# Kernel tuning notes

Measured on AMD Instinct MI355X. Metric: run time of the kernel, lower is better.

## Reference

```python
import jax, jax.numpy as jnp
import numpy as np

B, DIM, MID, H, W = 4, 256, 128, 128, 128
EPS = 1e-5


def _conv(x, w, pad):
    # x: [B,C,H,W], w: [O,I,k,k]
    return jax.lax.conv_general_dilated(
        x, w, window_strides=(1, 1), padding=[(pad, pad), (pad, pad)],
        dimension_numbers=('NCHW', 'OIHW', 'NCHW'))


def _bn(x, g, b, m, v):
    inv = jax.lax.rsqrt(v + EPS)
    scale = (g * inv)[None, :, None, None]
    shift = (b - m * g * inv)[None, :, None, None]
    return x * scale + shift


def _convbnrelu(x, w, g, b, m, v):
    return jax.nn.relu(_bn(_conv(x, w, 1), g, b, m, v))


# CornerNet directional pools: sequential max-accumulation scans.
def top_pool(x):     # max over y' >= y  -> reversed cummax along H
    return jax.lax.cummax(x, axis=2, reverse=True)

def bottom_pool(x):  # max over y' <= y
    return jax.lax.cummax(x, axis=2)

def left_pool(x):    # max over x' >= x
    return jax.lax.cummax(x, axis=3, reverse=True)

def right_pool(x):   # max over x' <= x
    return jax.lax.cummax(x, axis=3)


def setup_inputs() -> dict:
    key = jax.random.key(0)
    ks = jax.random.split(key, 32)
    it = iter(ks)

    def w(shape, scale=0.05):
        return jax.random.normal(next(it), shape, jnp.float32) * scale

    def bn_params(c):
        return (jnp.ones((c,), jnp.float32) + 0.1 * jax.random.normal(next(it), (c,), jnp.float32),
                0.1 * jax.random.normal(next(it), (c,), jnp.float32),
                0.1 * jax.random.normal(next(it), (c,), jnp.float32),
                jax.random.uniform(next(it), (c,), jnp.float32) + 0.5)

    inp = {'x': jax.random.normal(next(it), (B, DIM, H, W), jnp.float32)}

    inp['p1_w'] = w((MID, DIM, 3, 3))
    inp['p1_g'], inp['p1_b'], inp['p1_m'], inp['p1_v'] = bn_params(MID)
    inp['p2_w'] = w((MID, DIM, 3, 3))
    inp['p2_g'], inp['p2_b'], inp['p2_m'], inp['p2_v'] = bn_params(MID)
    inp['p_w'] = w((DIM, MID, 3, 3))
    inp['p_g'], inp['p_b'], inp['p_m'], inp['p_v'] = bn_params(DIM)
    inp['c1_w'] = w((DIM, DIM, 1, 1))
    inp['c1_g'], inp['c1_b'], inp['c1_m'], inp['c1_v'] = bn_params(DIM)
    inp['c2_w'] = w((DIM, DIM, 3, 3))
    inp['c2_g'], inp['c2_b'], inp['c2_m'], inp['c2_v'] = bn_params(DIM)
    return inp


def reference(x,
              p1_w, p1_g, p1_b, p1_m, p1_v,
              p2_w, p2_g, p2_b, p2_m, p2_v,
              p_w, p_g, p_b, p_m, p_v,
              c1_w, c1_g, c1_b, c1_m, c1_v,
              c2_w, c2_g, c2_b, c2_m, c2_v):
    # branch 1: conv-bn-relu -> top pool -> bottom pool
    pool1 = bottom_pool(top_pool(_convbnrelu(x, p1_w, p1_g, p1_b, p1_m, p1_v)))
    # branch 2: conv-bn-relu -> left pool -> right pool
    pool2 = right_pool(left_pool(_convbnrelu(x, p2_w, p2_g, p2_b, p2_m, p2_v)))
    # merge branch
    p_bn1 = _bn(_conv(pool1 + pool2, p_w, 1), p_g, p_b, p_m, p_v)
    # skip branch: 1x1 conv + bn
    bn1 = _bn(_conv(x, c1_w, 0), c1_g, c1_b, c1_m, c1_v)
    # residual add + relu, then final conv-bn-relu
    return _convbnrelu(jax.nn.relu(p_bn1 + bn1), c2_w, c2_g, c2_b, c2_m, c2_v)
```

## Files before the change

### kernel.cpp

```cpp
#include <hip/hip_runtime.h>
#include <hip/hip_bf16.h>
#include <math.h>


constexpr int NB   = 4;
constexpr int CDIM = 256;
constexpr int CMID = 128;
constexpr int HS   = 128;
constexpr int WS   = 128;
constexpr float EPS = 1e-5f;

typedef __bf16 bf16x8 __attribute__((ext_vector_type(8)));
typedef float  f32x4  __attribute__((ext_vector_type(4)));

#define AS1 __attribute__((address_space(1)))
#define AS3 __attribute__((address_space(3)))

__device__ __forceinline__ void load16_lds(const void* gsrc, void* ldst) {
    __builtin_amdgcn_global_load_lds((const AS1 unsigned int*)gsrc,
                                     (AS3 unsigned int*)ldst, 16, 0, 0);
}

__global__ __launch_bounds__(512) void k_xprep(const float* __restrict__ xin,
                                               __hip_bfloat16* __restrict__ Xc)
{
    const int y = blockIdx.x;
    const int b = blockIdx.y;
    const int t = threadIdx.x;
    __shared__ __hip_bfloat16 lds[128 * 264];
#pragma unroll
    for (int k = 0; k < 16; ++k) {
        int idx = t + k * 512;
        int ci = idx >> 5, x4 = idx & 31;
        f32x4 v = *(const f32x4*)(xin + (((size_t)b * CDIM + ci) * HS + y) * WS + x4 * 4);
#pragma unroll
        for (int j = 0; j < 4; ++j)
            lds[(x4 * 4 + j) * 264 + ci] = __float2bfloat16(v[j]);
    }
    __syncthreads();
#pragma unroll
    for (int k = 0; k < 8; ++k) {
        int i = t + k * 512;
        int x = i >> 5, c8 = i & 31;
        bf16x8 vv = *(const bf16x8*)(lds + x * 264 + c8 * 8);
        *(bf16x8*)(Xc + ((size_t)(b * 128 + y) * 128 + x) * 256 + c8 * 8) = vv;
    }
}

__global__ __launch_bounds__(256) void k_wprep_all(
    const float* __restrict__ p1w, const float* __restrict__ p2w,
    const float* __restrict__ c2w, const float* __restrict__ c1w,
    __hip_bfloat16* __restrict__ Aw1, __hip_bfloat16* __restrict__ Aw2,
    __hip_bfloat16* __restrict__ Aw5, __hip_bfloat16* __restrict__ Aw4,
    f32x4* __restrict__ zdst)
{
    const int bid = blockIdx.x;
    const int t   = threadIdx.x;
    if (bid < 512) {
        const float* W; __hip_bfloat16* A; int co;
        if (bid < 128)      { W = p1w; A = Aw1; co = bid; }
        else if (bid < 256) { W = p2w; A = Aw2; co = bid - 128; }
        else                { W = c2w; A = Aw5; co = bid - 256; }
#pragma unroll
        for (int tap = 0; tap < 9; ++tap)
            A[(size_t)co * 2304 + tap * 256 + t] =
                __float2bfloat16(W[((size_t)co * CDIM + t) * 9 + tap]);
    } else if (bid < 640) {
        int base = (bid - 512) * 512 + t;
        Aw4[base]       = __float2bfloat16(c1w[base]);
        Aw4[base + 256] = __float2bfloat16(c1w[base + 256]);
    } else if (bid < 768) {
        zdst[(size_t)(bid - 640) * 256 + t] = (f32x4){0.f, 0.f, 0.f, 0.f};
    } else {
        if (t < 16) zdst[32768 + t] = (f32x4){0.f, 0.f, 0.f, 0.f};
    }
}

template<int MODE>
__global__ __launch_bounds__(512, 2) void k_conv3(
    const __hip_bfloat16* __restrict__ Xc,
    const __hip_bfloat16* __restrict__ AwA, const __hip_bfloat16* __restrict__ AwB,
    const float* __restrict__ zbuf,
    const float* __restrict__ g1, const float* __restrict__ b1,
    const float* __restrict__ m1, const float* __restrict__ v1,
    const float* __restrict__ g2, const float* __restrict__ b2,
    const float* __restrict__ m2, const float* __restrict__ v2,
    float* __restrict__ out0, unsigned* __restrict__ cmax,
    unsigned* __restrict__ rmax, int CO)
{
    const int y0     = blockIdx.x * 4;
    const int branch = blockIdx.y;
    const int b      = blockIdx.z;
    const int co0    = (MODE == 0) ? branch * 128 : 0;

    const __hip_bfloat16* Aw = (MODE == 1 && branch) ? AwB : AwA;
    const float* gg  = (MODE == 1 && branch) ? g2 : g1;
    const float* bbp = (MODE == 1 && branch) ? b2 : b1;
    const float* mmp = (MODE == 1 && branch) ? m2 : m1;
    const float* vvp = (MODE == 1 && branch) ? v2 : v1;

    constexpr int BUFB = 904 * 64;
    __shared__ alignas(16) char smb[2 * BUFB];
    __shared__ float s_sc[128], s_sh[128];
    __shared__ unsigned s_red[4][128];

    const int t    = threadIdx.x;
    const int lane = t & 63;
    const int w    = t >> 6;
    const int ml   = lane & 15;
    const int q    = lane >> 4;
    const int yy    = w >> 1;
    const int mbase = (w & 1) * 64;

    if (t < 128) {
        int co = co0 + t;
        float iv = rsqrtf(vvp[co] + EPS);
        float sc = gg[co] * iv;
        s_sc[t] = sc;
        s_sh[t] = bbp[co] - mmp[co] * sc;
    }
    if (MODE == 1 && branch == 1) ((unsigned*)s_red)[t] = 0u;

    f32x4 acc[4][8];
#pragma unroll
    for (int mt = 0; mt < 4; ++mt)
#pragma unroll
        for (int nt = 0; nt < 8; ++nt)
            acc[mt][nt] = (f32x4){0.f, 0.f, 0.f, 0.f};

    const __hip_bfloat16* bbase = Xc + (size_t)(b * 128) * 128 * 256;

    auto stage_slot = [&](int p, int nky, int ncih, char* dst) {
        int i = t + p * 512;
        if (i < 3616) {
            int row = i >> 2, sl = i & 3;
            int c = sl ^ ((row >> 1) & 3);
            const __hip_bfloat16* src;
            if (row < 384) {
                int jj = row >> 7, col = row & 127;
                src = Aw + (size_t)(co0 + col) * 2304 + (3 * nky + jj) * 256
                         + ncih * 32 + c * 8;
            } else {
                int rbi = row - 384;
                int yl  = rbi / 130;
                int xi  = rbi - 130 * yl;
                int gy  = y0 + nky - 1 + yl, gx = xi - 1;
                src = ((unsigned)gy < 128u && (unsigned)gx < 128u)
                    ? bbase + ((size_t)(gy * 128 + gx)) * 256 + ncih * 32 + c * 8
                    : (const __hip_bfloat16*)((const char*)zbuf + c * 16);
            }
            load16_lds(src, dst + (size_t)i * 16);
        }
    };

#pragma unroll
    for (int p = 0; p < 8; ++p) stage_slot(p, 0, 0, smb);
    __syncthreads();

#pragma unroll 1
    for (int step = 0; step < 24; ++step) {
        const char* cb_ = smb + (size_t)(step & 1) * BUFB;
        char*       nb_ = smb + (size_t)((step + 1) & 1) * BUFB;
        const int nstep = step + 1;
        const int nky = nstep >> 3, ncih = nstep & 7;
        const bool last = (step == 23);

#pragma unroll
        for (int j = 0; j < 3; ++j) {
            bf16x8 af[4], bfv[8];
#pragma unroll
            for (int mt = 0; mt < 4; ++mt) {
                const int ra = j * 128 + mbase + mt * 16 + ml;
                const int sa = q ^ ((ra >> 1) & 3);
                af[mt] = *(const bf16x8*)(cb_ + (size_t)ra * 64 + sa * 16);
            }
#pragma unroll
            for (int nt = 0; nt < 8; ++nt) {
                const int rb = 384 + yy * 130 + nt * 16 + ml + j;
                const int sb = q ^ ((rb >> 1) & 3);
                bfv[nt] = *(const bf16x8*)(cb_ + (size_t)rb * 64 + sb * 16);
            }
            if (!last) {
                const int pbase = j * 3;
                const int pcnt  = (j == 2) ? 2 : 3;
#pragma unroll
                for (int pp = 0; pp < pcnt; ++pp)
                    stage_slot(pbase + pp, nky, ncih, nb_);
            }
            __builtin_amdgcn_s_barrier();
            __builtin_amdgcn_s_setprio(1);
#pragma unroll
            for (int mt = 0; mt < 4; ++mt)
#pragma unroll
                for (int nt = 0; nt < 8; ++nt)
                    acc[mt][nt] = __builtin_amdgcn_mfma_f32_16x16x32_bf16(
                        af[mt], bfv[nt], acc[mt][nt], 0, 0, 0);
            __builtin_amdgcn_s_setprio(0);
            __builtin_amdgcn_s_barrier();
        }
        __syncthreads();
    }

    if (MODE == 1 && branch == 0) {
        unsigned* colred = (unsigned*)smb;
#pragma unroll
        for (int k2 = 0; k2 < 32; ++k2) colred[t + k2 * 512] = 0u;
        __syncthreads();
    }

#pragma unroll
    for (int mt = 0; mt < 4; ++mt) {
#pragma unroll
        for (int r = 0; r < 4; ++r) {
            const int cl = mbase + mt * 16 + q * 4 + r;
            const float sc = s_sc[cl], sh = s_sh[cl];
            const int co = co0 + cl;
            unsigned rmx = 0u;
#pragma unroll
            for (int nt = 0; nt < 8; ++nt) {
                float va = fmaxf(acc[mt][nt][r] * sc + sh, 0.f);
                const int x = nt * 16 + ml;
                if (MODE == 0) {
                    out0[(((size_t)b * CO + co) * HS + y0 + yy) * WS + x] = va;
                } else if (branch == 0) {
                    atomicMax(((unsigned*)smb) + cl * 128 + x, __float_as_uint(va));
                } else {
                    rmx = max(rmx, __float_as_uint(va));
                }
            }
            if (MODE == 1 && branch == 1) atomicMax(&s_red[yy][cl], rmx);
        }
    }

    if (MODE == 1) {
        __syncthreads();
        if (branch == 0) {
            unsigned* colred = (unsigned*)smb;
#pragma unroll
            for (int k2 = 0; k2 < 32; ++k2) {
                int idx = t + k2 * 512;
                atomicMax(cmax + ((size_t)(b * 128 + (idx >> 7))) * 128 + (idx & 127),
                          colred[idx]);
            }
        } else {
            atomicMax(rmax + ((size_t)(b * 128 + (t & 127))) * 128 + y0 + (t >> 7),
                      s_red[t >> 7][t & 127]);
        }
    }
}

__global__ __launch_bounds__(128) void k_uv(
    const float* __restrict__ pw, const float* __restrict__ cm,
    const float* __restrict__ rm,
    __hip_bfloat16* __restrict__ U, __hip_bfloat16* __restrict__ V)
{
    const int co   = blockIdx.x;
    const int b    = blockIdx.y;
    const int mode = blockIdx.z;
    const int p    = threadIdx.x;
    float acc0 = 0.f, acc1 = 0.f, acc2 = 0.f;
    const float* base = (mode == 0) ? cm : rm;
    for (int ci = 0; ci < CMID; ++ci) {
        const float* w9 = pw + (co * CMID + ci) * 9;
        float s0[3], s1[3], s2[3];
        if (mode == 0) {
#pragma unroll
            for (int k = 0; k < 3; ++k) {
                float a = w9[k], qq = w9[3 + k], r = w9[6 + k];
                s0[k] = qq + r; s1[k] = a + qq + r; s2[k] = a + qq;
            }
        } else {
#pragma unroll
            for (int k = 0; k < 3; ++k) {
                float a = w9[k*3 + 0], qq = w9[k*3 + 1], r = w9[k*3 + 2];
                s0[k] = qq + r; s1[k] = a + qq + r; s2[k] = a + qq;
            }
        }
        const float* v = base + (b * CMID + ci) * 128;
#pragma unroll
        for (int k = 0; k < 3; ++k) {
            int pos = p + k - 1;
            if ((unsigned)pos < 128u) {
                float vv = v[pos];
                acc0 += s0[k] * vv; acc1 += s1[k] * vv; acc2 += s2[k] * vv;
            }
        }
    }
    __hip_bfloat16* dst = (mode == 0) ? U : V;
    dst[((0 * NB + b) * CDIM + co) * 128 + p] = __float2bfloat16(acc0);
    dst[((1 * NB + b) * CDIM + co) * 128 + p] = __float2bfloat16(acc1);
    dst[((2 * NB + b) * CDIM + co) * 128 + p] = __float2bfloat16(acc2);
}

__global__ __launch_bounds__(256, 2) void k_merge_mfma(
    const __hip_bfloat16* __restrict__ Xc, const __hip_bfloat16* __restrict__ Aw4,
    const __hip_bfloat16* __restrict__ U, const __hip_bfloat16* __restrict__ V,
    const float* __restrict__ pg, const float* __restrict__ pb,
    const float* __restrict__ pm, const float* __restrict__ pv,
    const float* __restrict__ cg, const float* __restrict__ cb,
    const float* __restrict__ cmn, const float* __restrict__ cv,
    __hip_bfloat16* __restrict__ Rc)
{
    const int y = blockIdx.x;
    const int b = blockIdx.y;
    __shared__ __hip_bfloat16 smem[32768];
    __shared__ float s_psc[256], s_psh[256], s_csc[256], s_csh[256];
    __shared__ float s_v0[256], s_vm[256], s_v1[256];
    char* smb = (char*)smem;
    const int t = threadIdx.x, lane = t & 63, w = t >> 6;
    const int ml = lane & 15, q = lane >> 4;
    const int mbase = w * 64;
    const int yc = (y == 0) ? 0 : ((y == HS - 1) ? 2 : 1);

    {
        int co = t;
        float iv = rsqrtf(pv[co] + EPS);
        float psc = pg[co] * iv;
        s_psc[co] = psc;
        s_psh[co] = pb[co] - pm[co] * psc;
        float iv2 = rsqrtf(cv[co] + EPS);
        float csc = cg[co] * iv2;
        s_csc[co] = csc;
        s_csh[co] = cb[co] - cmn[co] * csc;
        const size_t vb = ((size_t)b * CDIM + co) * 128 + y;
        const size_t cstr = (size_t)NB * CDIM * 128;
        s_v0[co] = __bfloat162float(V[vb]);
        s_vm[co] = __bfloat162float(V[cstr + vb]);
        s_v1[co] = __bfloat162float(V[2 * cstr + vb]);
    }

    f32x4 acc[4][8];
#pragma unroll
    for (int mt = 0; mt < 4; ++mt)
#pragma unroll
        for (int nt = 0; nt < 8; ++nt)
            acc[mt][nt] = (f32x4){0.f, 0.f, 0.f, 0.f};

    const __hip_bfloat16* brow = Xc + (size_t)(b * 128 + y) * 128 * 256;
#pragma unroll 1
    for (int ks = 0; ks < 4; ++ks) {
#pragma unroll
        for (int p = 0; p < 12; ++p) {
            int i   = t + p * 256;
            int row = i >> 3, sl = i & 7;
            int c   = sl ^ (row & 7);
            const __hip_bfloat16* src = (row < 256)
                ? Aw4 + (size_t)row * 256 + ks * 64 + c * 8
                : brow + (size_t)(row - 256) * 256 + ks * 64 + c * 8;
            load16_lds(src, smb + (size_t)i * 16);
        }
        __syncthreads();
#pragma unroll
        for (int s = 0; s < 2; ++s) {
            bf16x8 af[4], bfv[8];
#pragma unroll
            for (int mt = 0; mt < 4; ++mt) {
                const int ra = mbase + mt * 16 + ml;
                const int coff = ((s * 4 + q) ^ (ra & 7)) * 16;
                af[mt] = *(const bf16x8*)(smb + (size_t)ra * 128 + coff);
            }
#pragma unroll
            for (int nt = 0; nt < 8; ++nt) {
                const int rb = 256 + nt * 16 + ml;
                const int coff = ((s * 4 + q) ^ (rb & 7)) * 16;
                bfv[nt] = *(const bf16x8*)(smb + (size_t)rb * 128 + coff);
            }
#pragma unroll
            for (int mt = 0; mt < 4; ++mt)
#pragma unroll
                for (int nt = 0; nt < 8; ++nt)
                    acc[mt][nt] = __builtin_amdgcn_mfma_f32_16x16x32_bf16(
                        af[mt], bfv[nt], acc[mt][nt], 0, 0, 0);
        }
        __syncthreads();
    }

    const __hip_bfloat16* Ub = U + ((size_t)(yc * NB + b) * CDIM + mbase) * 128;
#pragma unroll
    for (int k = 0; k < 16; ++k) {
        int i = lane + k * 64;
        load16_lds(Ub + (size_t)i * 8, smb + (size_t)w * 16384 + (size_t)i * 16);
    }
    __syncthreads();
    const __hip_bfloat16* ulds = smem + w * 8192;

#pragma unroll
    for (int mt = 0; mt < 4; ++mt) {
#pragma unroll
        for (int nt = 0; nt < 8; ++nt) {
            const int x = nt * 16 + ml;
            unsigned long long pk = 0;
#pragma unroll
            for (int r = 0; r < 4; ++r) {
                const int cl = mt * 16 + q * 4 + r;
                const int co = mbase + cl;
                float u  = __bfloat162float(ulds[cl * 128 + x]);
                float vt = (x == 0) ? s_v0[co] : ((x == WS - 1) ? s_v1[co] : s_vm[co]);
                float val = fmaxf((u + vt) * s_psc[co] + s_psh[co]
                                  + acc[mt][nt][r] * s_csc[co] + s_csh[co], 0.f);
                __hip_bfloat16 hb = __float2bfloat16(val);
                unsigned short bits;
                __builtin_memcpy(&bits, &hb, 2);
                pk |= (unsigned long long)bits << (16 * r);
            }
            *(unsigned long long*)((char*)Rc +
                ((size_t)((b * 128 + y) * 128 + x) * 256 + mbase + mt * 16 + q * 4) * 2) = pk;
        }
    }
}

extern "C" void kernel_launch(void* const* d_in, const int* in_sizes, int n_in,
                              void* d_out, int out_size, void* d_ws, size_t ws_size,
                              hipStream_t stream)
{
    (void)in_sizes; (void)n_in; (void)out_size; (void)ws_size;
    const float* x    = (const float*)d_in[0];
    const float* p1_w = (const float*)d_in[1];
    const float* p1_g = (const float*)d_in[2];
    const float* p1_b = (const float*)d_in[3];
    const float* p1_m = (const float*)d_in[4];
    const float* p1_v = (const float*)d_in[5];
    const float* p2_w = (const float*)d_in[6];
    const float* p2_g = (const float*)d_in[7];
    const float* p2_b = (const float*)d_in[8];
    const float* p2_m = (const float*)d_in[9];
    const float* p2_v = (const float*)d_in[10];
    const float* p_w  = (const float*)d_in[11];
    const float* p_g  = (const float*)d_in[12];
    const float* p_b  = (const float*)d_in[13];
    const float* p_m  = (const float*)d_in[14];
    const float* p_v  = (const float*)d_in[15];
    const float* c1_w = (const float*)d_in[16];
    const float* c1_g = (const float*)d_in[17];
    const float* c1_b = (const float*)d_in[18];
    const float* c1_m = (const float*)d_in[19];
    const float* c1_v = (const float*)d_in[20];
    const float* c2_w = (const float*)d_in[21];
    const float* c2_g = (const float*)d_in[22];
    const float* c2_b = (const float*)d_in[23];
    const float* c2_m = (const float*)d_in[24];
    const float* c2_v = (const float*)d_in[25];
    float* out = (float*)d_out;
    char* ws = (char*)d_ws;

    __hip_bfloat16* Xc   = (__hip_bfloat16*)ws;
    __hip_bfloat16* Rc   = (__hip_bfloat16*)(ws + 33554432);
    __hip_bfloat16* Ubuf = (__hip_bfloat16*)(ws + 67108864);
    __hip_bfloat16* Vbuf = (__hip_bfloat16*)(ws + 67895296);
    __hip_bfloat16* Aw1  = (__hip_bfloat16*)(ws + 67108864);
    __hip_bfloat16* Aw2  = (__hip_bfloat16*)(ws + 67698688);
    __hip_bfloat16* Aw5  = (__hip_bfloat16*)(ws + 68681728);
    __hip_bfloat16* Aw4  = (__hip_bfloat16*)(ws + 69861376);
    unsigned*       cmaxU = (unsigned*)(ws + 69992448);
    unsigned*       rmaxU = (unsigned*)(ws + 70254592);
    float*          zbuf  = (float*)(ws + 70516736);

    k_wprep_all<<<dim3(769), 256, 0, stream>>>(
        p1_w, p2_w, c2_w, c1_w, Aw1, Aw2, Aw5, Aw4, (f32x4*)(ws + 69992448));
    k_xprep<<<dim3(128, 4), 512, 0, stream>>>(x, Xc);

    k_conv3<1><<<dim3(32, 2, 4), 512, 0, stream>>>(
        Xc, Aw1, Aw2, zbuf,
        p1_g, p1_b, p1_m, p1_v, p2_g, p2_b, p2_m, p2_v,
        nullptr, cmaxU, rmaxU, CMID);

    k_uv<<<dim3(256, 4, 2), 128, 0, stream>>>(
        p_w, (const float*)cmaxU, (const float*)rmaxU, Ubuf, Vbuf);

    k_merge_mfma<<<dim3(128, 4), 256, 0, stream>>>(
        Xc, Aw4, Ubuf, Vbuf, p_g, p_b, p_m, p_v,
        c1_g, c1_b, c1_m, c1_v, Rc);

    k_conv3<0><<<dim3(32, 2, 4), 512, 0, stream>>>(
        Rc, Aw5, nullptr, zbuf,
        c2_g, c2_b, c2_m, c2_v, nullptr, nullptr, nullptr, nullptr,
        out, nullptr, nullptr, CDIM);
}
```

Baseline: 397.3 us.

## Restructure conv staging: drop halo columns, fine-grained vmcnt waits, peeled last step

The shared-memory B tile no longer stores the two padding columns (128 rows per y instead of 130). Out-of-range x neighbours are now zeroed in registers after the LDS read. Staging is split into per-slot A and B loaders issued in a fixed order, so each phase waits only for the loads it needs via explicit vmcnt counts instead of full __syncthreads. The last K-step is peeled out to remove the per-iteration 'last' branch. This cuts LDS size and address math and overlaps loads more tightly with MFMA, at the cost of extra select instructions and reliance on exact vmcnt ordering for correctness.

```diff
diff --git a/kernel.cpp b/kernel.cpp
--- a/kernel.cpp
+++ b/kernel.cpp
@@ -99,7 +99,7 @@
     const float* mmp = (MODE == 1 && branch) ? m2 : m1;
     const float* vvp = (MODE == 1 && branch) ? v2 : v1;
 
-    constexpr int BUFB = 904 * 64;
+    constexpr int BUFB = 896 * 64;
     __shared__ alignas(16) char smb[2 * BUFB];
     __shared__ float s_sc[128], s_sh[128];
     __shared__ unsigned s_red[4][128];
@@ -112,6 +112,9 @@
     const int yy    = w >> 1;
     const int mbase = (w & 1) * 64;
 
+    const int cc  = (t & 3) ^ ((t >> 3) & 3);
+    const int col = t >> 2;
+
     if (t < 128) {
         int co = co0 + t;
         float iv = rsqrtf(vvp[co] + EPS);
@@ -129,77 +132,102 @@
             acc[mt][nt] = (f32x4){0.f, 0.f, 0.f, 0.f};
 
     const __hip_bfloat16* bbase = Xc + (size_t)(b * 128) * 128 * 256;
-
-    auto stage_slot = [&](int p, int nky, int ncih, char* dst) {
-        int i = t + p * 512;
-        if (i < 3616) {
-            int row = i >> 2, sl = i & 3;
-            int c = sl ^ ((row >> 1) & 3);
-            const __hip_bfloat16* src;
-            if (row < 384) {
-                int jj = row >> 7, col = row & 127;
-                src = Aw + (size_t)(co0 + col) * 2304 + (3 * nky + jj) * 256
-                         + ncih * 32 + c * 8;
-            } else {
-                int rbi = row - 384;
-                int yl  = rbi / 130;
-                int xi  = rbi - 130 * yl;
-                int gy  = y0 + nky - 1 + yl, gx = xi - 1;
-                src = ((unsigned)gy < 128u && (unsigned)gx < 128u)
-                    ? bbase + ((size_t)(gy * 128 + gx)) * 256 + ncih * 32 + c * 8
-                    : (const __hip_bfloat16*)((const char*)zbuf + c * 16);
-            }
-            load16_lds(src, dst + (size_t)i * 16);
-        }
+    const char* zrow = (const char*)zbuf + cc * 16;
+
+    auto stage_A = [&](char* dst, int p, int nky, int ncih) {
+        const __hip_bfloat16* src = Aw + (size_t)(co0 + col) * 2304
+            + (3 * nky + p) * 256 + ncih * 32 + cc * 8;
+        load16_lds(src, dst + (size_t)(t + p * 512) * 16);
     };
-
-#pragma unroll
-    for (int p = 0; p < 8; ++p) stage_slot(p, 0, 0, smb);
-    __syncthreads();
+    auto stage_B = [&](char* dst, int p, int nky, int ncih) {
+        const int gy = y0 + nky - 1 + (p - 3);
+        const __hip_bfloat16* src = ((unsigned)gy < 128u)
+            ? bbase + ((size_t)(gy * 128 + col)) * 256 + ncih * 32 + cc * 8
+            : (const __hip_bfloat16*)zrow;
+        load16_lds(src, dst + (size_t)(t + p * 512) * 16);
+    };
+
+    bf16x8 BZERO;
+#pragma unroll
+    for (int k = 0; k < 8; ++k) BZERO[k] = (__bf16)0.0f;
+
+    stage_B(smb, 3, 0, 0); stage_B(smb, 4, 0, 0); stage_B(smb, 5, 0, 0);
+    stage_B(smb, 6, 0, 0);
+    stage_A(smb, 0, 0, 0); stage_A(smb, 1, 0, 0); stage_A(smb, 2, 0, 0);
+
+#define WAITB(N) \
+    asm volatile("s_waitcnt vmcnt(" #N ")" ::: "memory"); \
+    __builtin_amdgcn_s_barrier(); \
+    __builtin_amdgcn_sched_barrier(0);
+
+#define DS_PHASE(J, CB) \
+    bf16x8 af[4], bfv[8]; \
+    { \
+        _Pragma("unroll") \
+        for (int mt = 0; mt < 4; ++mt) { \
+            const int ra = (J) * 128 + mbase + mt * 16 + ml; \
+            const int sa = q ^ ((ra >> 1) & 3); \
+            af[mt] = *(const bf16x8*)((CB) + (size_t)ra * 64 + sa * 16); \
+        } \
+        _Pragma("unroll") \
+        for (int nt = 0; nt < 8; ++nt) { \
+            const int rbl = nt * 16 + ml + (J) - 1; \
+            const int rbc = rbl < 0 ? 0 : (rbl > 127 ? 127 : rbl); \
+            const int rb  = 384 + yy * 128 + rbc; \
+            const int sb  = q ^ ((rb >> 1) & 3); \
+            bf16x8 bv = *(const bf16x8*)((CB) + (size_t)rb * 64 + sb * 16); \
+            bfv[nt] = ((unsigned)rbl < 128u) ? bv : BZERO; \
+        } \
+    }
+
+#define MFMA_PHASE() \
+    __builtin_amdgcn_s_setprio(1); \
+    _Pragma("unroll") \
+    for (int mt = 0; mt < 4; ++mt) \
+        _Pragma("unroll") \
+        for (int nt = 0; nt < 8; ++nt) \
+            acc[mt][nt] = __builtin_amdgcn_mfma_f32_16x16x32_bf16( \
+                af[mt], bfv[nt], acc[mt][nt], 0, 0, 0); \
+    __builtin_amdgcn_s_setprio(0);
 
 #pragma unroll 1
-    for (int step = 0; step < 24; ++step) {
+    for (int step = 0; step < 23; ++step) {
         const char* cb_ = smb + (size_t)(step & 1) * BUFB;
         char*       nb_ = smb + (size_t)((step + 1) & 1) * BUFB;
         const int nstep = step + 1;
         const int nky = nstep >> 3, ncih = nstep & 7;
-        const bool last = (step == 23);
-
-#pragma unroll
-        for (int j = 0; j < 3; ++j) {
-            bf16x8 af[4], bfv[8];
-#pragma unroll
-            for (int mt = 0; mt < 4; ++mt) {
-                const int ra = j * 128 + mbase + mt * 16 + ml;
-                const int sa = q ^ ((ra >> 1) & 3);
-                af[mt] = *(const bf16x8*)(cb_ + (size_t)ra * 64 + sa * 16);
-            }
-#pragma unroll
-            for (int nt = 0; nt < 8; ++nt) {
-                const int rb = 384 + yy * 130 + nt * 16 + ml + j;
-                const int sb = q ^ ((rb >> 1) & 3);
-                bfv[nt] = *(const bf16x8*)(cb_ + (size_t)rb * 64 + sb * 16);
-            }
-            if (!last) {
-                const int pbase = j * 3;
-                const int pcnt  = (j == 2) ? 2 : 3;
-#pragma unroll
-                for (int pp = 0; pp < pcnt; ++pp)
-                    stage_slot(pbase + pp, nky, ncih, nb_);
-            }
-            __builtin_amdgcn_s_barrier();
-            __builtin_amdgcn_s_setprio(1);
-#pragma unroll
-            for (int mt = 0; mt < 4; ++mt)
-#pragma unroll
-                for (int nt = 0; nt < 8; ++nt)
-                    acc[mt][nt] = __builtin_amdgcn_mfma_f32_16x16x32_bf16(
-                        af[mt], bfv[nt], acc[mt][nt], 0, 0, 0);
-            __builtin_amdgcn_s_setprio(0);
-            __builtin_amdgcn_s_barrier();
-        }
-        __syncthreads();
-    }
+        {
+            WAITB(2)
+            DS_PHASE(0, cb_)
+            stage_B(nb_, 3, nky, ncih);
+            stage_B(nb_, 4, nky, ncih);
+            stage_B(nb_, 5, nky, ncih);
+            MFMA_PHASE()
+        }
+        {
+            WAITB(4)
+            DS_PHASE(1, cb_)
+            stage_B(nb_, 6, nky, ncih);
+            stage_A(nb_, 0, nky, ncih);
+            MFMA_PHASE()
+        }
+        {
+            WAITB(5)
+            DS_PHASE(2, cb_)
+            stage_A(nb_, 1, nky, ncih);
+            stage_A(nb_, 2, nky, ncih);
+            MFMA_PHASE()
+        }
+    }
+    {
+        const char* cb_ = smb + BUFB;
+        { WAITB(2) DS_PHASE(0, cb_) MFMA_PHASE() }
+        { WAITB(1) DS_PHASE(1, cb_) MFMA_PHASE() }
+        { WAITB(0) DS_PHASE(2, cb_) MFMA_PHASE() }
+    }
+#undef WAITB
+#undef DS_PHASE
+#undef MFMA_PHASE
 
     if (MODE == 1 && branch == 0) {
         unsigned* colred = (unsigned*)smb;
```

New measurement: 388.3 us. 1.02x faster.

## Simplify conv staging: drop halo columns, fixed-slot loads, one barrier per step

Applied to the files above, without the earlier changes.

Replaces the generic per-slot staging lambda with dedicated A and B stagers. Each thread now loads fixed rows with no division or bounds branching. The B tile drops its 130-wide padded rows for 128-wide rows, and the x-direction zero padding is applied in registers by selecting a zero vector at the edges. All prefetch loads are issued once at the start of each step after a single vmcnt wait and barrier, replacing the interleaved per-j prefetches and two barriers per j. This cuts address arithmetic and barrier overhead, but adds per-fragment clamp and select logic and a full vmcnt(0) wait at each step start.

```diff
diff --git a/kernel.cpp b/kernel.cpp
--- a/kernel.cpp
+++ b/kernel.cpp
@@ -99,7 +99,7 @@
     const float* mmp = (MODE == 1 && branch) ? m2 : m1;
     const float* vvp = (MODE == 1 && branch) ? v2 : v1;
 
-    constexpr int BUFB = 904 * 64;
+    constexpr int BUFB = 896 * 64;
     __shared__ alignas(16) char smb[2 * BUFB];
     __shared__ float s_sc[128], s_sh[128];
     __shared__ unsigned s_red[4][128];
@@ -112,6 +112,9 @@
     const int yy    = w >> 1;
     const int mbase = (w & 1) * 64;
 
+    const int cc  = (t & 3) ^ ((t >> 3) & 3);
+    const int col = t >> 2;
+
     if (t < 128) {
         int co = co0 + t;
         float iv = rsqrtf(vvp[co] + EPS);
@@ -129,33 +132,28 @@
             acc[mt][nt] = (f32x4){0.f, 0.f, 0.f, 0.f};
 
     const __hip_bfloat16* bbase = Xc + (size_t)(b * 128) * 128 * 256;
-
-    auto stage_slot = [&](int p, int nky, int ncih, char* dst) {
-        int i = t + p * 512;
-        if (i < 3616) {
-            int row = i >> 2, sl = i & 3;
-            int c = sl ^ ((row >> 1) & 3);
-            const __hip_bfloat16* src;
-            if (row < 384) {
-                int jj = row >> 7, col = row & 127;
-                src = Aw + (size_t)(co0 + col) * 2304 + (3 * nky + jj) * 256
-                         + ncih * 32 + c * 8;
-            } else {
-                int rbi = row - 384;
-                int yl  = rbi / 130;
-                int xi  = rbi - 130 * yl;
-                int gy  = y0 + nky - 1 + yl, gx = xi - 1;
-                src = ((unsigned)gy < 128u && (unsigned)gx < 128u)
-                    ? bbase + ((size_t)(gy * 128 + gx)) * 256 + ncih * 32 + c * 8
-                    : (const __hip_bfloat16*)((const char*)zbuf + c * 16);
-            }
-            load16_lds(src, dst + (size_t)i * 16);
-        }
+    const char* zrow = (const char*)zbuf + cc * 16;
+
+    auto stage_A = [&](char* dst, int p, int nky, int ncih) {
+        const __hip_bfloat16* src = Aw + (size_t)(co0 + col) * 2304
+            + (3 * nky + p) * 256 + ncih * 32 + cc * 8;
+        load16_lds(src, dst + (size_t)(t + p * 512) * 16);
     };
-
-#pragma unroll
-    for (int p = 0; p < 8; ++p) stage_slot(p, 0, 0, smb);
-    __syncthreads();
+    auto stage_B = [&](char* dst, int p, int nky, int ncih) {
+        const int gy = y0 + nky - 1 + (p - 3);
+        const __hip_bfloat16* src = ((unsigned)gy < 128u)
+            ? bbase + ((size_t)(gy * 128 + col)) * 256 + ncih * 32 + cc * 8
+            : (const __hip_bfloat16*)zrow;
+        load16_lds(src, dst + (size_t)(t + p * 512) * 16);
+    };
+
+    bf16x8 BZERO;
+#pragma unroll
+    for (int k = 0; k < 8; ++k) BZERO[k] = (__bf16)0.0f;
+
+    stage_B(smb, 3, 0, 0); stage_B(smb, 4, 0, 0); stage_B(smb, 5, 0, 0);
+    stage_B(smb, 6, 0, 0);
+    stage_A(smb, 0, 0, 0); stage_A(smb, 1, 0, 0); stage_A(smb, 2, 0, 0);
 
 #pragma unroll 1
     for (int step = 0; step < 24; ++step) {
@@ -163,31 +161,39 @@
         char*       nb_ = smb + (size_t)((step + 1) & 1) * BUFB;
         const int nstep = step + 1;
         const int nky = nstep >> 3, ncih = nstep & 7;
-        const bool last = (step == 23);
-
-#pragma unroll
-        for (int j = 0; j < 3; ++j) {
+
+        asm volatile("s_waitcnt vmcnt(0)" ::: "memory");
+        __builtin_amdgcn_s_barrier();
+        __builtin_amdgcn_sched_barrier(0);
+
+        if (step < 23) {
+            stage_B(nb_, 3, nky, ncih);
+            stage_B(nb_, 4, nky, ncih);
+            stage_B(nb_, 5, nky, ncih);
+            stage_B(nb_, 6, nky, ncih);
+            stage_A(nb_, 0, nky, ncih);
+            stage_A(nb_, 1, nky, ncih);
+            stage_A(nb_, 2, nky, ncih);
+        }
+
+#pragma unroll
+        for (int J = 0; J < 3; ++J) {
             bf16x8 af[4], bfv[8];
 #pragma unroll
             for (int mt = 0; mt < 4; ++mt) {
-                const int ra = j * 128 + mbase + mt * 16 + ml;
+                const int ra = J * 128 + mbase + mt * 16 + ml;
                 const int sa = q ^ ((ra >> 1) & 3);
                 af[mt] = *(const bf16x8*)(cb_ + (size_t)ra * 64 + sa * 16);
             }
 #pragma unroll
             for (int nt = 0; nt < 8; ++nt) {
-                const int rb = 384 + yy * 130 + nt * 16 + ml + j;
-                const int sb = q ^ ((rb >> 1) & 3);
-                bfv[nt] = *(const bf16x8*)(cb_ + (size_t)rb * 64 + sb * 16);
-            }
-            if (!last) {
-                const int pbase = j * 3;
-                const int pcnt  = (j == 2) ? 2 : 3;
-#pragma unroll
-                for (int pp = 0; pp < pcnt; ++pp)
-                    stage_slot(pbase + pp, nky, ncih, nb_);
-            }
-            __builtin_amdgcn_s_barrier();
+                const int rbl = nt * 16 + ml + J - 1;
+                const int rbc = rbl < 0 ? 0 : (rbl > 127 ? 127 : rbl);
+                const int rb  = 384 + yy * 128 + rbc;
+                const int sb  = q ^ ((rb >> 1) & 3);
+                bf16x8 bv = *(const bf16x8*)(cb_ + (size_t)rb * 64 + sb * 16);
+                bfv[nt] = ((unsigned)rbl < 128u) ? bv : BZERO;
+            }
             __builtin_amdgcn_s_setprio(1);
 #pragma unroll
             for (int mt = 0; mt < 4; ++mt)
@@ -196,9 +202,7 @@
                     acc[mt][nt] = __builtin_amdgcn_mfma_f32_16x16x32_bf16(
                         af[mt], bfv[nt], acc[mt][nt], 0, 0, 0);
             __builtin_amdgcn_s_setprio(0);
-            __builtin_amdgcn_s_barrier();
-        }
-        __syncthreads();
+        }
     }
 
     if (MODE == 1 && branch == 0) {
```

After: 404.6 us. About the same (+1.9%).
